# Kernel tuning notes

Hardware: AMD Instinct MI355X
Metric: run time of the kernel (lower is better)

## Reference

```python
import jax, jax.numpy as jnp
import numpy as np

B, S, D, H = 32, 578, 1024, 16  # seq = (384//16)**2 + 2 = 578
DH = D // H  # 64, per-head size
INIT_STD = 0.02


def setup_inputs() -> dict:
    key = jax.random.key(0)
    ks = jax.random.split(key, 7)
    hidden_states = jax.random.normal(ks[0], (B, S, D), dtype=jnp.float32)
    # Per-head Dense layers: stack H separate [D, DH] kernels -> [H, D, DH]
    Wq = jax.random.normal(ks[1], (H, D, DH), dtype=jnp.float32) * INIT_STD
    Wk = jax.random.normal(ks[2], (H, D, DH), dtype=jnp.float32) * INIT_STD
    Wv = jax.random.normal(ks[3], (H, D, DH), dtype=jnp.float32) * INIT_STD
    bq = jax.random.normal(ks[4], (H, DH), dtype=jnp.float32) * INIT_STD
    bk = jax.random.normal(ks[5], (H, DH), dtype=jnp.float32) * INIT_STD
    bv = jax.random.normal(ks[6], (H, DH), dtype=jnp.float32) * INIT_STD
    return {"hidden_states": hidden_states, "Wq": Wq, "bq": bq,
            "Wk": Wk, "bk": bk, "Wv": Wv, "bv": bv}


def reference(hidden_states, Wq, bq, Wk, bk, Wv, bv):
    # Per-head Dense projections (original: Python list of H Dense layers),
    # expressed as one batched einsum over the head axis.
    # hidden_states: [B, S, D]; W*: [H, D, E]; b*: [H, E]
    q = jnp.einsum('bsd,hde->bhse', hidden_states, Wq) + bq[None, :, None, :]
    k = jnp.einsum('bsd,hde->bhse', hidden_states, Wk) + bk[None, :, None, :]
    v = jnp.einsum('bsd,hde->bhse', hidden_states, Wv) + bv[None, :, None, :]
    scale = 1.0 / jnp.sqrt(jnp.asarray(DH, dtype=q.dtype))
    scores = jnp.einsum('bhse,bhte->bhst', q, k) * scale  # [B, H, S, S]
    probs = jax.nn.softmax(scores, axis=-1)  # stable_softmax; dropout p=0
    out = jnp.einsum('bhst,bhte->bhse', probs, v)  # [B, H, S, E]
    # concat heads along last axis -> [B, S, H*E]
    return out.transpose(0, 2, 1, 3).reshape(B, S, H * DH)
```

## Files before the change

kernel.cpp:

```cpp
#include <hip/hip_runtime.h>

typedef __attribute__((ext_vector_type(8))) short short8;
typedef __attribute__((ext_vector_type(4))) float f32x4;
typedef unsigned short u16;
typedef unsigned int u32;

#define B_ 32
#define S_ 578
#define D_ 1024
#define H_ 16
#define DH_ 64
#define M_ 18496
#define MP2_ 18688
#define N_ 3072
#define K_ 1024
#define ST_ 640
#define BHROWS_ (B_ * H_ * S_ + 64)
#define SCALE2 0.18033688011112042f
#define CMAX 16.0f

__device__ __forceinline__ u16 f2bf(float x) {
  u32 u = __float_as_uint(x);
  u = (u + 0x7fffu + ((u >> 16) & 1u)) >> 16;
  return (u16)u;
}

__device__ __forceinline__ void gload_lds16(const u16* g, u16* l) {
  __builtin_amdgcn_global_load_lds((const __attribute__((address_space(1))) void*)g,
                                   (__attribute__((address_space(3))) void*)l, 16, 0, 0);
}

__global__ __launch_bounds__(256) void cvt_hidden(const float* __restrict__ in, u16* __restrict__ o) {
  long i = ((long)blockIdx.x * 256 + threadIdx.x) * 8;
  if (i >= (long)M_ * D_) {
    short8 z = {0, 0, 0, 0, 0, 0, 0, 0};
    *(short8*)(o + i) = z;
    return;
  }
  float4 f0 = *(const float4*)(in + i);
  float4 f1 = *(const float4*)(in + i + 4);
  short8 v;
  u16* p = (u16*)&v;
  p[0] = f2bf(f0.x); p[1] = f2bf(f0.y); p[2] = f2bf(f0.z); p[3] = f2bf(f0.w);
  p[4] = f2bf(f1.x); p[5] = f2bf(f1.y); p[6] = f2bf(f1.z); p[7] = f2bf(f1.w);
  *(short8*)(o + i) = v;
}

__global__ __launch_bounds__(256) void wt_kernel(const float* __restrict__ Wq, const float* __restrict__ Wk,
                                                 const float* __restrict__ Wv, u16* __restrict__ Wt) {
  const int d0 = blockIdx.x * 64;
  const int h = blockIdx.y;
  const int qkv = blockIdx.z;
  const float* W = (qkv == 0) ? Wq : ((qkv == 1) ? Wk : Wv);
  __shared__ float tile[64][65];
  const int t = threadIdx.x;
  {
    int e = t & 63, dr = t >> 6;
#pragma unroll
    for (int p = 0; p < 16; ++p) {
      int dd = dr + p * 4;
      tile[dd][e] = W[((long)h * D_ + d0 + dd) * DH_ + e];
    }
  }
  __syncthreads();
  {
    int dd = t & 63, er = t >> 6;
#pragma unroll
    for (int p = 0; p < 16; ++p) {
      int ee = er + p * 4;
      long n = (long)qkv * 1024 + h * 64 + ee;
      Wt[n * K_ + d0 + dd] = f2bf(tile[dd][ee]);
    }
  }
}

__global__ __launch_bounds__(256) void bias_kernel(const float* __restrict__ bq, const float* __restrict__ bk,
                                                   const float* __restrict__ bv, float* __restrict__ bias) {
  int i = blockIdx.x * 256 + threadIdx.x;
  if (i < 3072) {
    const float* src = (i < 1024) ? bq : ((i < 2048) ? bk : bv);
    bias[i] = src[i & 1023];
  }
}


__device__ __forceinline__ void stage256(const u16* __restrict__ g, u16* l, int tid, int k0) {
  const int r = tid >> 2;
  const int gch = (tid & 3) ^ ((tid >> 3) & 3);
  const u16* src = g + (long)r * K_ + k0 + gch * 8;
  gload_lds16(src, l + tid * 8);
  gload_lds16(src + 128L * K_, l + 4096 + tid * 8);
}

template <int CUR, int NX2, bool STG, int VM>
__device__ __forceinline__ void tile_step(const u16* __restrict__ Ag, const u16* __restrict__ Bg,
                                          u16 (*Abuf)[256 * 32], u16 (*Bbuf)[256 * 32],
                                          f32x4 (&acc)[8][4], int tid, int arow, int brow, int sw, int k2) {
  const short8* Av = (const short8*)Abuf[CUR];
  const short8* Bv = (const short8*)Bbuf[CUR];
  if constexpr (STG) stage256(Ag, Abuf[NX2], tid, k2);
  if constexpr (VM == 6) asm volatile("s_waitcnt vmcnt(6)" ::: "memory");
  else if constexpr (VM == 4) asm volatile("s_waitcnt vmcnt(4)" ::: "memory");
  else asm volatile("s_waitcnt vmcnt(0)" ::: "memory");
  __builtin_amdgcn_s_barrier();
  __builtin_amdgcn_sched_barrier(0);
  short8 a[8], b0, b1;
#pragma unroll
  for (int mi = 0; mi < 8; ++mi) a[mi] = Av[(arow + mi * 16) * 4 + sw];
  b0 = Bv[brow * 4 + sw];
  b1 = Bv[(brow + 16) * 4 + sw];
  asm volatile("s_waitcnt lgkmcnt(0)" ::: "memory");
  __builtin_amdgcn_sched_barrier(0);
  __builtin_amdgcn_s_setprio(1);
#pragma unroll
  for (int mi = 0; mi < 8; ++mi) {
    acc[mi][0] = __builtin_amdgcn_mfma_f32_16x16x32_bf16(a[mi], b0, acc[mi][0], 0, 0, 0);
    acc[mi][1] = __builtin_amdgcn_mfma_f32_16x16x32_bf16(a[mi], b1, acc[mi][1], 0, 0, 0);
  }
  __builtin_amdgcn_s_setprio(0);
  __builtin_amdgcn_s_barrier();
  __builtin_amdgcn_sched_barrier(0);
  if constexpr (STG) stage256(Bg, Bbuf[NX2], tid, k2);
  short8 b2 = Bv[(brow + 32) * 4 + sw];
  short8 b3 = Bv[(brow + 48) * 4 + sw];
  asm volatile("s_waitcnt lgkmcnt(0)" ::: "memory");
  __builtin_amdgcn_sched_barrier(0);
  __builtin_amdgcn_s_setprio(1);
#pragma unroll
  for (int mi = 0; mi < 8; ++mi) {
    acc[mi][2] = __builtin_amdgcn_mfma_f32_16x16x32_bf16(a[mi], b2, acc[mi][2], 0, 0, 0);
    acc[mi][3] = __builtin_amdgcn_mfma_f32_16x16x32_bf16(a[mi], b3, acc[mi][3], 0, 0, 0);
  }
  __builtin_amdgcn_s_setprio(0);
  __builtin_amdgcn_s_barrier();
  __builtin_amdgcn_sched_barrier(0);
}

__global__ __launch_bounds__(512, 2) void qkv_gemm(const u16* __restrict__ A, const u16* __restrict__ Bt,
                                                   const float* __restrict__ bias,
                                                   u16* __restrict__ qb, u16* __restrict__ kb,
                                                   u16* __restrict__ vbt) {
  __shared__ alignas(16) u16 Abuf[3][256 * 32];
  __shared__ alignas(16) u16 Bbuf[3][256 * 32];
  const int tid = threadIdx.x, wid = tid >> 6, lane = tid & 63, quad = lane >> 4, l16 = lane & 15;
  const int wr = wid >> 2, wc = wid & 3;

  const int nwg = 73 * 12;
  const int qq = nwg >> 3, rr = nwg & 7;
  int xcd = blockIdx.x & 7, loc = blockIdx.x >> 3;
  int wg = (xcd < rr ? xcd * (qq + 1) : rr * (qq + 1) + (xcd - rr) * qq) + loc;
  const int mt = wg / 12, nt = wg - mt * 12;
  const long m0 = (long)mt * 256, n0 = (long)nt * 256;
  const u16* Ag = A + m0 * K_;
  const u16* Bg = Bt + n0 * K_;

  f32x4 acc[8][4];
#pragma unroll
  for (int mi = 0; mi < 8; ++mi)
#pragma unroll
    for (int ni = 0; ni < 4; ++ni) { f32x4 z = {0.f, 0.f, 0.f, 0.f}; acc[mi][ni] = z; }

  const int sw = quad ^ ((l16 >> 1) & 3);
  const int arow = wr * 128 + l16;
  const int brow = wc * 64 + l16;

  stage256(Ag, Abuf[0], tid, 0);
  stage256(Bg, Bbuf[0], tid, 0);
  stage256(Ag, Abuf[1], tid, 32);
  stage256(Bg, Bbuf[1], tid, 32);

#pragma unroll 1
  for (int t = 0; t < 30; t += 3) {
    tile_step<0, 2, true, 6>(Ag, Bg, Abuf, Bbuf, acc, tid, arow, brow, sw, (t + 2) * 32);
    tile_step<1, 0, true, 6>(Ag, Bg, Abuf, Bbuf, acc, tid, arow, brow, sw, (t + 3) * 32);
    tile_step<2, 1, true, 6>(Ag, Bg, Abuf, Bbuf, acc, tid, arow, brow, sw, (t + 4) * 32);
  }
  tile_step<0, 2, false, 4>(Ag, Bg, Abuf, Bbuf, acc, tid, arow, brow, sw, 0);
  tile_step<1, 0, false, 0>(Ag, Bg, Abuf, Bbuf, acc, tid, arow, brow, sw, 0);

  const long nb = n0 + wc * 64;
  const int h = (int)((nb >> 6) & 15);
  const int qkvsel = (int)(nb >> 10);
  float bv4[4];
#pragma unroll
  for (int ni = 0; ni < 4; ++ni) bv4[ni] = bias[nb + ni * 16 + l16];

  if (qkvsel == 2) {
#pragma unroll
    for (int mi = 0; mi < 8; ++mi) {
#pragma unroll
      for (int r = 0; r < 4; ++r) {
        long m = m0 + wr * 128 + mi * 16 + quad * 4 + r;
        if (m < M_) {
          unsigned bi = (unsigned)m / (unsigned)S_;
          unsigned si = (unsigned)m - bi * (unsigned)S_;
          long base = ((long)(bi * H_ + h) * DH_) * ST_ + si;
#pragma unroll
          for (int ni = 0; ni < 4; ++ni) {
            float v = acc[mi][ni][r] + bv4[ni];
            vbt[base + (long)(ni * 16 + l16) * ST_] = f2bf(v);
          }
        }
      }
    }
  } else {
    u16* dst = (qkvsel == 0) ? qb : kb;
#pragma unroll
    for (int mi = 0; mi < 8; ++mi) {
#pragma unroll
      for (int r = 0; r < 4; ++r) {
        long m = m0 + wr * 128 + mi * 16 + quad * 4 + r;
        if (m < M_) {
          unsigned bi = (unsigned)m / (unsigned)S_;
          unsigned si = (unsigned)m - bi * (unsigned)S_;
          long base = ((long)(bi * H_ + h) * S_ + si) * DH_;
#pragma unroll
          for (int ni = 0; ni < 4; ++ni) {
            float v = acc[mi][ni][r] + bv4[ni];
            dst[base + ni * 16 + l16] = f2bf(v);
          }
        }
      }
    }
  }
}

__global__ __launch_bounds__(256) void attn_kernel(const u16* __restrict__ qb, const u16* __restrict__ kb,
                                                   const u16* __restrict__ vbt, float* __restrict__ out) {
  __shared__ alignas(16) u16 Ks[64 * 64];
  __shared__ alignas(16) u16 Vs[64 * 64];
  __shared__ alignas(16) u16 Ps[4 * 16 * 72];
  const int tid = threadIdx.x, wave = tid >> 6, lane = tid & 63, quad = lane >> 4, l16 = lane & 15;
  const int qt = blockIdx.x, h = blockIdx.y, b = blockIdx.z;
  const long bh = (long)b * H_ + h;
  const u16* qp = qb + bh * S_ * DH_;
  const u16* kp = kb + bh * S_ * DH_;
  const u16* vtp = vbt + bh * DH_ * ST_;
  const int q0 = qt * 64;

  short8 qf0, qf1;
  {
    int row = q0 + wave * 16 + l16;
    const short8* qv = (const short8*)(qp + (long)row * DH_);
    qf0 = qv[quad];
    qf1 = qv[4 + quad];
  }

  f32x4 O[4];
#pragma unroll
  for (int et = 0; et < 4; ++et) { f32x4 z = {0.f, 0.f, 0.f, 0.f}; O[et] = z; }
  float lp[4] = {0.f, 0.f, 0.f, 0.f};

  const int srow0 = tid >> 3;
  const int slot = tid & 7;
  const int s0 = quad ^ (l16 & 7);

  for (int kt = 0; kt < 10; ++kt) {
    const int t0 = kt * 64;
    __syncthreads();
#pragma unroll
    for (int p = 0; p < 2; ++p) {
      int row = srow0 + 32 * p;
      int gch = slot ^ (row & 7);
      gload_lds16(kp + (long)(t0 + row) * DH_ + gch * 8, &Ks[(tid + 256 * p) * 8]);
      gload_lds16(vtp + (long)row * ST_ + t0 + gch * 8, &Vs[(tid + 256 * p) * 8]);
    }
    __syncthreads();

    float p[4][4];
    const short8* Kv8 = (const short8*)Ks;
#pragma unroll
    for (int jt = 0; jt < 4; ++jt) {
      f32x4 sacc = {0.f, 0.f, 0.f, 0.f};
      short8 kf0 = Kv8[(16 * jt + l16) * 8 + s0];
      short8 kf1 = Kv8[(16 * jt + l16) * 8 + ((quad + 4) ^ (l16 & 7))];
      sacc = __builtin_amdgcn_mfma_f32_16x16x32_bf16(qf0, kf0, sacc, 0, 0, 0);
      sacc = __builtin_amdgcn_mfma_f32_16x16x32_bf16(qf1, kf1, sacc, 0, 0, 0);
      bool valid = (t0 + 16 * jt + l16) < S_;
#pragma unroll
      for (int r = 0; r < 4; ++r) {
        float e = valid ? exp2f(sacc[r] * SCALE2 - CMAX) : 0.f;
        p[jt][r] = e;
        lp[r] += e;
      }
    }

    u16* Pw = Ps + wave * 16 * 72;
#pragma unroll
    for (int jt = 0; jt < 4; ++jt)
#pragma unroll
      for (int r = 0; r < 4; ++r)
        Pw[(quad * 4 + r) * 72 + 16 * jt + l16] = f2bf(p[jt][r]);

    const short8* Pv8 = (const short8*)(Ps + wave * 16 * 72);
    const short8* Vv8 = (const short8*)Vs;
#pragma unroll
    for (int ks = 0; ks < 2; ++ks) {
      short8 pa = Pv8[l16 * 9 + ks * 4 + quad];
#pragma unroll
      for (int et = 0; et < 4; ++et) {
        short8 vf = Vv8[(16 * et + l16) * 8 + ((ks * 4 + quad) ^ (l16 & 7))];
        O[et] = __builtin_amdgcn_mfma_f32_16x16x32_bf16(pa, vf, O[et], 0, 0, 0);
      }
    }
  }

  float inv[4];
#pragma unroll
  for (int r = 0; r < 4; ++r) {
    float s = lp[r];
    s += __shfl_xor(s, 1);
    s += __shfl_xor(s, 2);
    s += __shfl_xor(s, 4);
    s += __shfl_xor(s, 8);
    inv[r] = 1.0f / s;
  }
#pragma unroll
  for (int et = 0; et < 4; ++et)
#pragma unroll
    for (int r = 0; r < 4; ++r) {
      int s = q0 + wave * 16 + quad * 4 + r;
      if (s < S_) out[((long)b * S_ + s) * (H_ * DH_) + (long)h * DH_ + et * 16 + l16] = O[et][r] * inv[r];
    }
}

extern "C" void kernel_launch(void* const* d_in, const int* in_sizes, int n_in,
                              void* d_out, int out_size, void* d_ws, size_t ws_size,
                              hipStream_t stream) {
  const float* hs = (const float*)d_in[0];
  const float* Wq = (const float*)d_in[1];
  const float* bq = (const float*)d_in[2];
  const float* Wk = (const float*)d_in[3];
  const float* bk = (const float*)d_in[4];
  const float* Wv = (const float*)d_in[5];
  const float* bv = (const float*)d_in[6];
  float* out = (float*)d_out;

  u16* Abf = (u16*)d_ws;
  u16* Wt = Abf + (size_t)MP2_ * K_;
  float* bias = (float*)(Wt + (size_t)N_ * K_);
  u16* qb = (u16*)(bias + N_);
  u16* kb = qb + (size_t)BHROWS_ * DH_;
  u16* vbt = kb + (size_t)BHROWS_ * DH_;

  cvt_hidden<<<dim3(9344), dim3(256), 0, stream>>>(hs, Abf);
  wt_kernel<<<dim3(16, 16, 3), dim3(256), 0, stream>>>(Wq, Wk, Wv, Wt);
  bias_kernel<<<dim3(12), dim3(256), 0, stream>>>(bq, bk, bv, bias);
  qkv_gemm<<<dim3(876), dim3(512), 0, stream>>>(Abf, Wt, bias, qb, kb, vbt);
  attn_kernel<<<dim3(10, 16, 32), dim3(256), 0, stream>>>(qb, kb, vbt, out);
}
```

Before: 454.7 us.

## Restructure QKV GEMM pipeline to double-buffered 64-wide K steps

Replaces the triple-buffered 32-wide K pipeline with a double-buffered scheme where each step handles two 32-wide K slabs (64 of K total). Global-to-LDS staging of the next buffer is interleaved among the four MFMA phases, and the vmcnt waits are moved to the ends of the phases. The aim is fewer barriers and waits per unit of K and more overlap of loads with MFMA work, at the cost of more LDS and a schedule that is more complex and easier to get subtly wrong.

```diff
diff --git a/kernel.cpp b/kernel.cpp
--- a/kernel.cpp
+++ b/kernel.cpp
@@ -84,7 +84,7 @@
 }
 
 
-__device__ __forceinline__ void stage256(const u16* __restrict__ g, u16* l, int tid, int k0) {
+__device__ __forceinline__ void stage_slab(const u16* __restrict__ g, u16* l, int tid, int k0) {
   const int r = tid >> 2;
   const int gch = (tid & 3) ^ ((tid >> 3) & 3);
   const u16* src = g + (long)r * K_ + k0 + gch * 8;
@@ -92,23 +92,22 @@
   gload_lds16(src + 128L * K_, l + 4096 + tid * 8);
 }
 
-template <int CUR, int NX2, bool STG, int VM>
+template <int CUR, bool STG, int V2, int V4>
 __device__ __forceinline__ void tile_step(const u16* __restrict__ Ag, const u16* __restrict__ Bg,
-                                          u16 (*Abuf)[256 * 32], u16 (*Bbuf)[256 * 32],
+                                          u16 (*Ab)[2][8192], u16 (*Bb)[2][8192],
                                           f32x4 (&acc)[8][4], int tid, int arow, int brow, int sw, int k2) {
-  const short8* Av = (const short8*)Abuf[CUR];
-  const short8* Bv = (const short8*)Bbuf[CUR];
-  if constexpr (STG) stage256(Ag, Abuf[NX2], tid, k2);
-  if constexpr (VM == 6) asm volatile("s_waitcnt vmcnt(6)" ::: "memory");
-  else if constexpr (VM == 4) asm volatile("s_waitcnt vmcnt(4)" ::: "memory");
-  else asm volatile("s_waitcnt vmcnt(0)" ::: "memory");
-  __builtin_amdgcn_s_barrier();
-  __builtin_amdgcn_sched_barrier(0);
-  short8 a[8], b0, b1;
-#pragma unroll
-  for (int mi = 0; mi < 8; ++mi) a[mi] = Av[(arow + mi * 16) * 4 + sw];
-  b0 = Bv[brow * 4 + sw];
-  b1 = Bv[(brow + 16) * 4 + sw];
+  const short8* Av0 = (const short8*)Ab[CUR][0];
+  const short8* Av1 = (const short8*)Ab[CUR][1];
+  const short8* Bv0 = (const short8*)Bb[CUR][0];
+  const short8* Bv1 = (const short8*)Bb[CUR][1];
+  short8 a[8], b0, b1, b2, b3;
+
+#pragma unroll
+  for (int mi = 0; mi < 8; ++mi) a[mi] = Av0[(arow + mi * 16) * 4 + sw];
+  b0 = Bv0[brow * 4 + sw];
+  b1 = Bv0[(brow + 16) * 4 + sw];
+  if constexpr (STG) stage_slab(Ag, &Ab[CUR ^ 1][0][0], tid, k2);
+  __builtin_amdgcn_s_barrier();
   asm volatile("s_waitcnt lgkmcnt(0)" ::: "memory");
   __builtin_amdgcn_sched_barrier(0);
   __builtin_amdgcn_s_setprio(1);
@@ -120,9 +119,11 @@
   __builtin_amdgcn_s_setprio(0);
   __builtin_amdgcn_s_barrier();
   __builtin_amdgcn_sched_barrier(0);
-  if constexpr (STG) stage256(Bg, Bbuf[NX2], tid, k2);
-  short8 b2 = Bv[(brow + 32) * 4 + sw];
-  short8 b3 = Bv[(brow + 48) * 4 + sw];
+
+  b2 = Bv0[(brow + 32) * 4 + sw];
+  b3 = Bv0[(brow + 48) * 4 + sw];
+  if constexpr (STG) stage_slab(Bg, &Bb[CUR ^ 1][0][0], tid, k2);
+  __builtin_amdgcn_s_barrier();
   asm volatile("s_waitcnt lgkmcnt(0)" ::: "memory");
   __builtin_amdgcn_sched_barrier(0);
   __builtin_amdgcn_s_setprio(1);
@@ -132,6 +133,43 @@
     acc[mi][3] = __builtin_amdgcn_mfma_f32_16x16x32_bf16(a[mi], b3, acc[mi][3], 0, 0, 0);
   }
   __builtin_amdgcn_s_setprio(0);
+  if constexpr (V2 == 4) asm volatile("s_waitcnt vmcnt(4)" ::: "memory");
+  else if constexpr (V2 == 0) asm volatile("s_waitcnt vmcnt(0)" ::: "memory");
+  __builtin_amdgcn_s_barrier();
+  __builtin_amdgcn_sched_barrier(0);
+
+#pragma unroll
+  for (int mi = 0; mi < 8; ++mi) a[mi] = Av1[(arow + mi * 16) * 4 + sw];
+  b0 = Bv1[brow * 4 + sw];
+  b1 = Bv1[(brow + 16) * 4 + sw];
+  if constexpr (STG) stage_slab(Ag, &Ab[CUR ^ 1][1][0], tid, k2 + 32);
+  __builtin_amdgcn_s_barrier();
+  asm volatile("s_waitcnt lgkmcnt(0)" ::: "memory");
+  __builtin_amdgcn_sched_barrier(0);
+  __builtin_amdgcn_s_setprio(1);
+#pragma unroll
+  for (int mi = 0; mi < 8; ++mi) {
+    acc[mi][0] = __builtin_amdgcn_mfma_f32_16x16x32_bf16(a[mi], b0, acc[mi][0], 0, 0, 0);
+    acc[mi][1] = __builtin_amdgcn_mfma_f32_16x16x32_bf16(a[mi], b1, acc[mi][1], 0, 0, 0);
+  }
+  __builtin_amdgcn_s_setprio(0);
+  __builtin_amdgcn_s_barrier();
+  __builtin_amdgcn_sched_barrier(0);
+
+  b2 = Bv1[(brow + 32) * 4 + sw];
+  b3 = Bv1[(brow + 48) * 4 + sw];
+  if constexpr (STG) stage_slab(Bg, &Bb[CUR ^ 1][1][0], tid, k2 + 32);
+  __builtin_amdgcn_s_barrier();
+  asm volatile("s_waitcnt lgkmcnt(0)" ::: "memory");
+  __builtin_amdgcn_sched_barrier(0);
+  __builtin_amdgcn_s_setprio(1);
+#pragma unroll
+  for (int mi = 0; mi < 8; ++mi) {
+    acc[mi][2] = __builtin_amdgcn_mfma_f32_16x16x32_bf16(a[mi], b2, acc[mi][2], 0, 0, 0);
+    acc[mi][3] = __builtin_amdgcn_mfma_f32_16x16x32_bf16(a[mi], b3, acc[mi][3], 0, 0, 0);
+  }
+  __builtin_amdgcn_s_setprio(0);
+  if constexpr (V4 == 4) asm volatile("s_waitcnt vmcnt(4)" ::: "memory");
   __builtin_amdgcn_s_barrier();
   __builtin_amdgcn_sched_barrier(0);
 }
@@ -140,8 +178,8 @@
                                                    const float* __restrict__ bias,
                                                    u16* __restrict__ qb, u16* __restrict__ kb,
                                                    u16* __restrict__ vbt) {
-  __shared__ alignas(16) u16 Abuf[3][256 * 32];
-  __shared__ alignas(16) u16 Bbuf[3][256 * 32];
+  __shared__ alignas(16) u16 Ab[2][2][8192];
+  __shared__ alignas(16) u16 Bb[2][2][8192];
   const int tid = threadIdx.x, wid = tid >> 6, lane = tid & 63, quad = lane >> 4, l16 = lane & 15;
   const int wr = wid >> 2, wc = wid & 3;
 
@@ -164,19 +202,21 @@
   const int arow = wr * 128 + l16;
   const int brow = wc * 64 + l16;
 
-  stage256(Ag, Abuf[0], tid, 0);
-  stage256(Bg, Bbuf[0], tid, 0);
-  stage256(Ag, Abuf[1], tid, 32);
-  stage256(Bg, Bbuf[1], tid, 32);
+  stage_slab(Ag, &Ab[0][0][0], tid, 0);
+  stage_slab(Bg, &Bb[0][0][0], tid, 0);
+  stage_slab(Ag, &Ab[0][1][0], tid, 32);
+  stage_slab(Bg, &Bb[0][1][0], tid, 32);
+  asm volatile("s_waitcnt vmcnt(4)" ::: "memory");
+  __builtin_amdgcn_s_barrier();
+  __builtin_amdgcn_sched_barrier(0);
 
 #pragma unroll 1
-  for (int t = 0; t < 30; t += 3) {
-    tile_step<0, 2, true, 6>(Ag, Bg, Abuf, Bbuf, acc, tid, arow, brow, sw, (t + 2) * 32);
-    tile_step<1, 0, true, 6>(Ag, Bg, Abuf, Bbuf, acc, tid, arow, brow, sw, (t + 3) * 32);
-    tile_step<2, 1, true, 6>(Ag, Bg, Abuf, Bbuf, acc, tid, arow, brow, sw, (t + 4) * 32);
-  }
-  tile_step<0, 2, false, 4>(Ag, Bg, Abuf, Bbuf, acc, tid, arow, brow, sw, 0);
-  tile_step<1, 0, false, 0>(Ag, Bg, Abuf, Bbuf, acc, tid, arow, brow, sw, 0);
+  for (int t = 0; t < 14; t += 2) {
+    tile_step<0, true, 4, 4>(Ag, Bg, Ab, Bb, acc, tid, arow, brow, sw, (t + 1) * 64);
+    tile_step<1, true, 4, 4>(Ag, Bg, Ab, Bb, acc, tid, arow, brow, sw, (t + 2) * 64);
+  }
+  tile_step<0, true, 4, 4>(Ag, Bg, Ab, Bb, acc, tid, arow, brow, sw, 15 * 64);
+  tile_step<1, false, 0, -1>(Ag, Bg, Ab, Bb, acc, tid, arow, brow, sw, 0);
 
   const long nb = n0 + wc * 64;
   const int h = (int)((nb >> 6) & 15);
```

Result: no change. 462.5 us (+1.7%).

## Halve QKV GEMM M-tile and replace triple-buffered pipeline with double buffering

Applied to the files above, without the earlier changes.

The QKV projection GEMM now uses 128x256 output tiles instead of 256x256, which doubles the grid to 1752 workgroups and simplifies the XCD-aware block remap. The hand-scheduled three-stage LDS pipeline (explicit vmcnt waits, split B loads, setprio) is replaced by a plain two-stage double buffer synchronised with __syncthreads. Launch bounds now request 4 blocks per CU. The aim is higher occupancy and better latency hiding through more resident waves. In exchange, each tile reuses its B data across fewer rows, and the fine-grained overlap of loads with MFMA is lost. The LDS footprint per block may also limit how many blocks actually fit on a CU.

```diff
diff --git a/kernel.cpp b/kernel.cpp
--- a/kernel.cpp
+++ b/kernel.cpp
@@ -84,7 +84,13 @@
 }
 
 
-__device__ __forceinline__ void stage256(const u16* __restrict__ g, u16* l, int tid, int k0) {
+__device__ __forceinline__ void stage_a(const u16* __restrict__ g, u16* l, int tid, int k0) {
+  const int r = tid >> 2;
+  const int gch = (tid & 3) ^ ((tid >> 3) & 3);
+  gload_lds16(g + (long)r * K_ + k0 + gch * 8, l + tid * 8);
+}
+
+__device__ __forceinline__ void stage_b(const u16* __restrict__ g, u16* l, int tid, int k0) {
   const int r = tid >> 2;
   const int gch = (tid & 3) ^ ((tid >> 3) & 3);
   const u16* src = g + (long)r * K_ + k0 + gch * 8;
@@ -92,91 +98,74 @@
   gload_lds16(src + 128L * K_, l + 4096 + tid * 8);
 }
 
-template <int CUR, int NX2, bool STG, int VM>
-__device__ __forceinline__ void tile_step(const u16* __restrict__ Ag, const u16* __restrict__ Bg,
-                                          u16 (*Abuf)[256 * 32], u16 (*Bbuf)[256 * 32],
-                                          f32x4 (&acc)[8][4], int tid, int arow, int brow, int sw, int k2) {
-  const short8* Av = (const short8*)Abuf[CUR];
-  const short8* Bv = (const short8*)Bbuf[CUR];
-  if constexpr (STG) stage256(Ag, Abuf[NX2], tid, k2);
-  if constexpr (VM == 6) asm volatile("s_waitcnt vmcnt(6)" ::: "memory");
-  else if constexpr (VM == 4) asm volatile("s_waitcnt vmcnt(4)" ::: "memory");
-  else asm volatile("s_waitcnt vmcnt(0)" ::: "memory");
-  __builtin_amdgcn_s_barrier();
-  __builtin_amdgcn_sched_barrier(0);
-  short8 a[8], b0, b1;
-#pragma unroll
-  for (int mi = 0; mi < 8; ++mi) a[mi] = Av[(arow + mi * 16) * 4 + sw];
-  b0 = Bv[brow * 4 + sw];
-  b1 = Bv[(brow + 16) * 4 + sw];
-  asm volatile("s_waitcnt lgkmcnt(0)" ::: "memory");
-  __builtin_amdgcn_sched_barrier(0);
-  __builtin_amdgcn_s_setprio(1);
-#pragma unroll
-  for (int mi = 0; mi < 8; ++mi) {
-    acc[mi][0] = __builtin_amdgcn_mfma_f32_16x16x32_bf16(a[mi], b0, acc[mi][0], 0, 0, 0);
-    acc[mi][1] = __builtin_amdgcn_mfma_f32_16x16x32_bf16(a[mi], b1, acc[mi][1], 0, 0, 0);
-  }
-  __builtin_amdgcn_s_setprio(0);
-  __builtin_amdgcn_s_barrier();
-  __builtin_amdgcn_sched_barrier(0);
-  if constexpr (STG) stage256(Bg, Bbuf[NX2], tid, k2);
-  short8 b2 = Bv[(brow + 32) * 4 + sw];
-  short8 b3 = Bv[(brow + 48) * 4 + sw];
-  asm volatile("s_waitcnt lgkmcnt(0)" ::: "memory");
-  __builtin_amdgcn_sched_barrier(0);
-  __builtin_amdgcn_s_setprio(1);
-#pragma unroll
-  for (int mi = 0; mi < 8; ++mi) {
-    acc[mi][2] = __builtin_amdgcn_mfma_f32_16x16x32_bf16(a[mi], b2, acc[mi][2], 0, 0, 0);
-    acc[mi][3] = __builtin_amdgcn_mfma_f32_16x16x32_bf16(a[mi], b3, acc[mi][3], 0, 0, 0);
-  }
-  __builtin_amdgcn_s_setprio(0);
-  __builtin_amdgcn_s_barrier();
-  __builtin_amdgcn_sched_barrier(0);
-}
-
-__global__ __launch_bounds__(512, 2) void qkv_gemm(const u16* __restrict__ A, const u16* __restrict__ Bt,
+__global__ __launch_bounds__(512, 4) void qkv_gemm(const u16* __restrict__ A, const u16* __restrict__ Bt,
                                                    const float* __restrict__ bias,
                                                    u16* __restrict__ qb, u16* __restrict__ kb,
                                                    u16* __restrict__ vbt) {
-  __shared__ alignas(16) u16 Abuf[3][256 * 32];
-  __shared__ alignas(16) u16 Bbuf[3][256 * 32];
+  __shared__ alignas(16) u16 Ab[2][128 * 32];
+  __shared__ alignas(16) u16 Bb[2][256 * 32];
   const int tid = threadIdx.x, wid = tid >> 6, lane = tid & 63, quad = lane >> 4, l16 = lane & 15;
   const int wr = wid >> 2, wc = wid & 3;
 
-  const int nwg = 73 * 12;
-  const int qq = nwg >> 3, rr = nwg & 7;
-  int xcd = blockIdx.x & 7, loc = blockIdx.x >> 3;
-  int wg = (xcd < rr ? xcd * (qq + 1) : rr * (qq + 1) + (xcd - rr) * qq) + loc;
+  const int wg = (blockIdx.x & 7) * 219 + (blockIdx.x >> 3);
   const int mt = wg / 12, nt = wg - mt * 12;
-  const long m0 = (long)mt * 256, n0 = (long)nt * 256;
+  const long m0 = (long)mt * 128, n0 = (long)nt * 256;
   const u16* Ag = A + m0 * K_;
   const u16* Bg = Bt + n0 * K_;
 
-  f32x4 acc[8][4];
-#pragma unroll
-  for (int mi = 0; mi < 8; ++mi)
+  f32x4 acc[4][4];
+#pragma unroll
+  for (int mi = 0; mi < 4; ++mi)
 #pragma unroll
     for (int ni = 0; ni < 4; ++ni) { f32x4 z = {0.f, 0.f, 0.f, 0.f}; acc[mi][ni] = z; }
 
   const int sw = quad ^ ((l16 >> 1) & 3);
-  const int arow = wr * 128 + l16;
+  const int arow = wr * 64 + l16;
   const int brow = wc * 64 + l16;
 
-  stage256(Ag, Abuf[0], tid, 0);
-  stage256(Bg, Bbuf[0], tid, 0);
-  stage256(Ag, Abuf[1], tid, 32);
-  stage256(Bg, Bbuf[1], tid, 32);
+  stage_a(Ag, Ab[0], tid, 0);
+  stage_b(Bg, Bb[0], tid, 0);
+  __syncthreads();
 
 #pragma unroll 1
-  for (int t = 0; t < 30; t += 3) {
-    tile_step<0, 2, true, 6>(Ag, Bg, Abuf, Bbuf, acc, tid, arow, brow, sw, (t + 2) * 32);
-    tile_step<1, 0, true, 6>(Ag, Bg, Abuf, Bbuf, acc, tid, arow, brow, sw, (t + 3) * 32);
-    tile_step<2, 1, true, 6>(Ag, Bg, Abuf, Bbuf, acc, tid, arow, brow, sw, (t + 4) * 32);
-  }
-  tile_step<0, 2, false, 4>(Ag, Bg, Abuf, Bbuf, acc, tid, arow, brow, sw, 0);
-  tile_step<1, 0, false, 0>(Ag, Bg, Abuf, Bbuf, acc, tid, arow, brow, sw, 0);
+  for (int t = 0; t < 32; t += 2) {
+    {
+      stage_a(Ag, Ab[1], tid, (t + 1) * 32);
+      stage_b(Bg, Bb[1], tid, (t + 1) * 32);
+      const short8* Av = (const short8*)Ab[0];
+      const short8* Bv = (const short8*)Bb[0];
+      short8 a[4], b[4];
+#pragma unroll
+      for (int mi = 0; mi < 4; ++mi) a[mi] = Av[(arow + mi * 16) * 4 + sw];
+#pragma unroll
+      for (int ni = 0; ni < 4; ++ni) b[ni] = Bv[(brow + ni * 16) * 4 + sw];
+#pragma unroll
+      for (int mi = 0; mi < 4; ++mi)
+#pragma unroll
+        for (int ni = 0; ni < 4; ++ni)
+          acc[mi][ni] = __builtin_amdgcn_mfma_f32_16x16x32_bf16(a[mi], b[ni], acc[mi][ni], 0, 0, 0);
+      __syncthreads();
+    }
+    {
+      if (t + 2 < 32) {
+        stage_a(Ag, Ab[0], tid, (t + 2) * 32);
+        stage_b(Bg, Bb[0], tid, (t + 2) * 32);
+      }
+      const short8* Av = (const short8*)Ab[1];
+      const short8* Bv = (const short8*)Bb[1];
+      short8 a[4], b[4];
+#pragma unroll
+      for (int mi = 0; mi < 4; ++mi) a[mi] = Av[(arow + mi * 16) * 4 + sw];
+#pragma unroll
+      for (int ni = 0; ni < 4; ++ni) b[ni] = Bv[(brow + ni * 16) * 4 + sw];
+#pragma unroll
+      for (int mi = 0; mi < 4; ++mi)
+#pragma unroll
+        for (int ni = 0; ni < 4; ++ni)
+          acc[mi][ni] = __builtin_amdgcn_mfma_f32_16x16x32_bf16(a[mi], b[ni], acc[mi][ni], 0, 0, 0);
+      __syncthreads();
+    }
+  }
 
   const long nb = n0 + wc * 64;
   const int h = (int)((nb >> 6) & 15);
@@ -187,10 +176,10 @@
 
   if (qkvsel == 2) {
 #pragma unroll
-    for (int mi = 0; mi < 8; ++mi) {
+    for (int mi = 0; mi < 4; ++mi) {
 #pragma unroll
       for (int r = 0; r < 4; ++r) {
-        long m = m0 + wr * 128 + mi * 16 + quad * 4 + r;
+        long m = m0 + wr * 64 + mi * 16 + quad * 4 + r;
         if (m < M_) {
           unsigned bi = (unsigned)m / (unsigned)S_;
           unsigned si = (unsigned)m - bi * (unsigned)S_;
@@ -206,10 +195,10 @@
   } else {
     u16* dst = (qkvsel == 0) ? qb : kb;
 #pragma unroll
-    for (int mi = 0; mi < 8; ++mi) {
+    for (int mi = 0; mi < 4; ++mi) {
 #pragma unroll
       for (int r = 0; r < 4; ++r) {
-        long m = m0 + wr * 128 + mi * 16 + quad * 4 + r;
+        long m = m0 + wr * 64 + mi * 16 + quad * 4 + r;
         if (m < M_) {
           unsigned bi = (unsigned)m / (unsigned)S_;
           unsigned si = (unsigned)m - bi * (unsigned)S_;
@@ -346,6 +335,6 @@
   cvt_hidden<<<dim3(9344), dim3(256), 0, stream>>>(hs, Abf);
   wt_kernel<<<dim3(16, 16, 3), dim3(256), 0, stream>>>(Wq, Wk, Wv, Wt);
   bias_kernel<<<dim3(12), dim3(256), 0, stream>>>(bq, bk, bv, bias);
-  qkv_gemm<<<dim3(876), dim3(512), 0, stream>>>(Abf, Wt, bias, qb, kb, vbt);
+  qkv_gemm<<<dim3(1752), dim3(512), 0, stream>>>(Abf, Wt, bias, qb, kb, vbt);
   attn_kernel<<<dim3(10, 16, 32), dim3(256), 0, stream>>>(qb, kb, vbt, out);
 }
```

After: 451.8 us. About the same (-0.6%).
